# Optimization experiments

Hardware: AMD Instinct MI355X
Metric: run time of the kernel (lower is better)

Reference implementation:

```python
import jax, jax.numpy as jnp
import numpy as np

B, L, D, N, R = 8, 4096, 768, 16, 8

def setup_inputs() -> dict:
    key = jax.random.key(0)
    ks = jax.random.split(key, 12)
    return {
        "x": jax.random.normal(ks[0], (B, L, D), jnp.float32),
        "a_logit": jnp.zeros((N,), jnp.float32),
        "U": jax.random.normal(ks[1], (N, R), jnp.float32) * 0.02,
        "V": jax.random.normal(ks[2], (N, R), jnp.float32) * 0.02,
        "W_in": jax.random.normal(ks[3], (N, D), jnp.float32) * (1.0 / np.sqrt(D)),
        "b_in": jax.random.normal(ks[4], (N,), jnp.float32) * 0.02,
        "W_gate": jax.random.normal(ks[5], (N, D), jnp.float32) * (1.0 / np.sqrt(D)),
        "b_gate": jax.random.normal(ks[6], (N,), jnp.float32) * 0.02,
        "W_out": jax.random.normal(ks[7], (D, N), jnp.float32) * (1.0 / np.sqrt(N)),
        "b_out": jax.random.normal(ks[8], (D,), jnp.float32) * 0.02,
        "W_skip": jax.random.normal(ks[9], (D, D), jnp.float32) * (1.0 / np.sqrt(D)),
        "b_skip": jax.random.normal(ks[10], (D,), jnp.float32) * 0.02,
    }

def reference(x, a_logit, U, V, W_in, b_in, W_gate, b_gate, W_out, b_out, W_skip, b_skip):
    # x: [B, L, D]
    u = jnp.einsum('bld,nd->bln', x, W_in) + b_in            # [B, L, N]
    g = jax.nn.sigmoid(jnp.einsum('bld,nd->bln', x, W_gate) + b_gate)
    a = jax.nn.sigmoid(a_logit)                              # [N]
    lowrank_T = V @ U.T                                      # (U @ V.T).T, [N, N]
    gu = g * u                                               # [B, L, N]

    def step(h, gu_t):
        # h: [B, N]; h_new = a*h + g_t*u_t + h @ lowrank.T
        h = h * a + gu_t + h @ lowrank_T
        return h, h

    h0 = jnp.zeros((x.shape[0], a_logit.shape[0]), x.dtype)
    _, hs = jax.lax.scan(step, h0, jnp.swapaxes(gu, 0, 1))   # hs: [L, B, N]
    hs = jnp.swapaxes(hs, 0, 1)                              # [B, L, N]
    # batched out_proj + skip across all timesteps
    y = jnp.einsum('bln,dn->bld', hs, W_out) + b_out \
        + jnp.einsum('ble,de->bld', x, W_skip) + b_skip
    return y
```

## Files before the change

kernel.cpp:

```cpp
#include <hip/hip_runtime.h>
#include <hip/hip_bf16.h>
#include <math.h>

#define BB 8
#define LL 4096
#define DD 768
#define NN 16
#define RR 8
#define MROWS (BB*LL)
#define KAUG 800
#define CCH 64
#define NCH (LL/CCH)

typedef unsigned int u32;
typedef unsigned short u16;
typedef __attribute__((ext_vector_type(8))) short short8;
typedef __attribute__((ext_vector_type(4))) float f32x4;
typedef __attribute__((ext_vector_type(4))) unsigned short us4;

__device__ __forceinline__ u16 f2bf(float f) {
  u32 u = __float_as_uint(f);
  u32 r = (u + 0x7fffu + ((u >> 16) & 1u)) >> 16;
  return (u16)r;
}

__device__ __forceinline__ void gload_lds16(const void* g, void* l) {
  __builtin_amdgcn_global_load_lds(
      (const __attribute__((address_space(1))) u32*)g,
      (__attribute__((address_space(3))) u32*)l, 16, 0, 0);
}

__global__ void k_prep(const float* __restrict__ a_logit, const float* __restrict__ U,
                       const float* __restrict__ V, const float* __restrict__ b_out,
                       const float* __restrict__ b_skip,
                       float* __restrict__ Mw, float* __restrict__ MCw,
                       float* __restrict__ bsum) {
  __shared__ float cur[256];
  __shared__ float nxt[256];
  int t = threadIdx.x;
  int m = t >> 4, n = t & 15;
  float s = 0.f;
  #pragma unroll
  for (int r = 0; r < RR; r++) s += V[m*RR+r] * U[n*RR+r];
  if (m == n) s += 1.f / (1.f + expf(-a_logit[n]));
  cur[t] = s;
  Mw[t] = s;
  __syncthreads();
  for (int it = 0; it < 6; ++it) {
    float acc = 0.f;
    #pragma unroll
    for (int k = 0; k < 16; k++) acc += cur[m*16+k] * cur[k*16+n];
    nxt[t] = acc;
    __syncthreads();
    cur[t] = nxt[t];
    __syncthreads();
  }
  MCw[t] = cur[t];
  for (int d = t; d < DD; d += 256) bsum[d] = b_out[d] + b_skip[d];
}

__global__ void k_weights(const float* __restrict__ W_skip, const float* __restrict__ W_out,
                          const float* __restrict__ W_in, const float* __restrict__ W_gate,
                          u16* __restrict__ Waug, u16* __restrict__ WinG) {
  int bid = blockIdx.x;
  int t = threadIdx.x;
  if (bid < DD) {
    int d = bid;
    for (int c = t; c < KAUG; c += 256) {
      float v;
      if (c < DD)           v = W_skip[d*DD + c];
      else if (c < DD+NN)   v = W_out[d*NN + (c-DD)];
      else                  v = 0.f;
      Waug[d*KAUG + c] = f2bf(v);
    }
  } else {
    int r = bid - DD;
    const float* Wsrc = (r < NN) ? (W_in + r*DD) : (W_gate + (r-NN)*DD);
    for (int c = t; c < DD; c += 256) WinG[r*DD + c] = f2bf(Wsrc[c]);
  }
}

__global__ void k_convert(const float* __restrict__ x, u16* __restrict__ Xaug) {
  const long total4 = (long)MROWS * (DD/4);
  const int stride = gridDim.x * blockDim.x;
  for (long i = (long)blockIdx.x*blockDim.x + threadIdx.x; i < total4; i += stride) {
    long row = i / (DD/4);
    int  c4  = (int)(i - row*(DD/4));
    float4 v = ((const float4*)x)[i];
    us4 o;
    o.x = f2bf(v.x); o.y = f2bf(v.y); o.z = f2bf(v.z); o.w = f2bf(v.w);
    *(us4*)(Xaug + row*KAUG + c4*4) = o;
  }
  const long totalz = (long)MROWS * 4;
  for (long i = (long)blockIdx.x*blockDim.x + threadIdx.x; i < totalz; i += stride) {
    long row = i >> 2; int q = (int)(i & 3);
    us4 z = (us4)0;
    *(us4*)(Xaug + row*KAUG + 784 + q*4) = z;
  }
}

__global__ __launch_bounds__(256) void k_gu(const u16* __restrict__ Xaug,
                                            const u16* __restrict__ WinG,
                                            const float* __restrict__ b_in,
                                            const float* __restrict__ b_gate,
                                            float* __restrict__ gu) {
  __shared__ u16 At[128*32];
  __shared__ u16 Bt[32*32];
  int tid = threadIdx.x;
  int wave = tid >> 6, lane = tid & 63;
  int rowbase = blockIdx.x * 128;
  f32x4 acc[2][2] = {};
  for (int it = 0; it < DD/32; ++it) {
    int k0 = it * 32;
    #pragma unroll
    for (int p = 0; p < 2; p++) {
      int c = tid + p*256;
      int r = c >> 2, co = c & 3;
      gload_lds16(Xaug + (long)(rowbase + r)*KAUG + k0 + co*8, At + c*8);
    }
    if (tid < 128) {
      int r = tid >> 2, co = tid & 3;
      gload_lds16(WinG + r*DD + k0 + co*8, Bt + tid*8);
    }
    __syncthreads();
    int l15 = lane & 15, lh = lane >> 4;
    short8 a[2], b[2];
    #pragma unroll
    for (int i = 0; i < 2; i++)
      a[i] = *(const short8*)(At + (wave*32 + i*16 + l15)*32 + lh*8);
    #pragma unroll
    for (int j = 0; j < 2; j++)
      b[j] = *(const short8*)(Bt + (j*16 + l15)*32 + lh*8);
    #pragma unroll
    for (int i = 0; i < 2; i++)
      #pragma unroll
      for (int j = 0; j < 2; j++)
        acc[i][j] = __builtin_amdgcn_mfma_f32_16x16x32_bf16(a[i], b[j], acc[i][j], 0, 0, 0);
    __syncthreads();
  }
  int l15 = lane & 15, lh = lane >> 4;
  float bi = b_in[l15], bg = b_gate[l15];
  #pragma unroll
  for (int i = 0; i < 2; i++)
    #pragma unroll
    for (int r = 0; r < 4; r++) {
      int row = rowbase + wave*32 + i*16 + lh*4 + r;
      float u = acc[i][0][r] + bi;
      float g = 1.f / (1.f + __expf(-(acc[i][1][r] + bg)));
      gu[(long)row*NN + l15] = g * u;
    }
}

__global__ void k_scan_local(const float* __restrict__ gu, const float* __restrict__ Mw,
                             float* __restrict__ cend) {
  int lane = threadIdx.x & 63;
  int grp = lane >> 4, n = lane & 15;
  int cid = blockIdx.x*4 + grp;
  int b = cid >> 6, k = cid & 63;
  float Mcol[16];
  #pragma unroll
  for (int m = 0; m < 16; m++) Mcol[m] = Mw[m*16 + n];
  float h = 0.f;
  const float* g = gu + ((long)(b*LL) + k*CCH)*NN + n;
  for (int t = 0; t < CCH; t++) {
    float hn = g[(long)t*NN];
    #pragma unroll
    for (int m = 0; m < 16; m++) hn += __shfl(h, m, 16) * Mcol[m];
    h = hn;
  }
  cend[(b*NCH + k)*NN + n] = h;
}

__global__ void k_scan_prefix(const float* __restrict__ cend, const float* __restrict__ MCw,
                              float* __restrict__ Hstart) {
  int t = threadIdx.x;
  int b = t >> 4, n = t & 15;
  float Mcol[16];
  #pragma unroll
  for (int m = 0; m < 16; m++) Mcol[m] = MCw[m*16 + n];
  float h = 0.f;
  for (int k = 0; k < NCH; k++) {
    Hstart[(b*NCH + k)*NN + n] = h;
    float hn = cend[(b*NCH + k)*NN + n];
    #pragma unroll
    for (int m = 0; m < 16; m++) hn += __shfl(h, m, 16) * Mcol[m];
    h = hn;
  }
}

__global__ void k_scan_final(const float* __restrict__ gu, const float* __restrict__ Mw,
                             const float* __restrict__ Hstart, u16* __restrict__ Xaug) {
  int lane = threadIdx.x & 63;
  int grp = lane >> 4, n = lane & 15;
  int cid = blockIdx.x*4 + grp;
  int b = cid >> 6, k = cid & 63;
  float Mcol[16];
  #pragma unroll
  for (int m = 0; m < 16; m++) Mcol[m] = Mw[m*16 + n];
  float h = Hstart[(b*NCH + k)*NN + n];
  const float* g = gu + ((long)(b*LL) + k*CCH)*NN + n;
  u16* xa = Xaug + ((long)(b*LL) + k*CCH)*KAUG + DD + n;
  for (int t = 0; t < CCH; t++) {
    float hn = g[(long)t*NN];
    #pragma unroll
    for (int m = 0; m < 16; m++) hn += __shfl(h, m, 16) * Mcol[m];
    h = hn;
    xa[(long)t*KAUG] = f2bf(h);
  }
}

__global__ __launch_bounds__(256) void k_out(const u16* __restrict__ Xaug,
                                             const u16* __restrict__ Waug,
                                             const float* __restrict__ bsum,
                                             float* __restrict__ y) {
  __shared__ u16 At[128*32];
  __shared__ u16 Bt[128*32];
  int tid = threadIdx.x;
  int wave = tid >> 6, lane = tid & 63;
  int wm = wave >> 1, wn = wave & 1;
  int rowbase = blockIdx.x * 128;
  int colbase = blockIdx.y * 128;
  f32x4 acc[4][4] = {};
  for (int it = 0; it < KAUG/32; ++it) {
    int k0 = it * 32;
    #pragma unroll
    for (int p = 0; p < 2; p++) {
      int c = tid + p*256;
      int r = c >> 2, co = c & 3;
      gload_lds16(Xaug + (long)(rowbase + r)*KAUG + k0 + co*8, At + c*8);
      gload_lds16(Waug + (long)(colbase + r)*KAUG + k0 + co*8, Bt + c*8);
    }
    __syncthreads();
    int l15 = lane & 15, lh = lane >> 4;
    short8 a[4], b[4];
    #pragma unroll
    for (int i = 0; i < 4; i++)
      a[i] = *(const short8*)(At + (wm*64 + i*16 + l15)*32 + lh*8);
    #pragma unroll
    for (int j = 0; j < 4; j++)
      b[j] = *(const short8*)(Bt + (wn*64 + j*16 + l15)*32 + lh*8);
    #pragma unroll
    for (int i = 0; i < 4; i++)
      #pragma unroll
      for (int j = 0; j < 4; j++)
        acc[i][j] = __builtin_amdgcn_mfma_f32_16x16x32_bf16(a[i], b[j], acc[i][j], 0, 0, 0);
    __syncthreads();
  }
  int l15 = lane & 15, lh = lane >> 4;
  #pragma unroll
  for (int j = 0; j < 4; j++) {
    int col = colbase + wn*64 + j*16 + l15;
    float bs = bsum[col];
    #pragma unroll
    for (int i = 0; i < 4; i++) {
      int row0 = rowbase + wm*64 + i*16 + lh*4;
      #pragma unroll
      for (int r = 0; r < 4; r++)
        y[(long)(row0 + r)*DD + col] = acc[i][j][r] + bs;
    }
  }
}

extern "C" void kernel_launch(void* const* d_in, const int* in_sizes, int n_in,
                              void* d_out, int out_size, void* d_ws, size_t ws_size,
                              hipStream_t stream) {
  (void)in_sizes; (void)n_in; (void)out_size; (void)ws_size;
  const float* x       = (const float*)d_in[0];
  const float* a_logit = (const float*)d_in[1];
  const float* U       = (const float*)d_in[2];
  const float* V       = (const float*)d_in[3];
  const float* W_in    = (const float*)d_in[4];
  const float* b_in    = (const float*)d_in[5];
  const float* W_gate  = (const float*)d_in[6];
  const float* b_gate  = (const float*)d_in[7];
  const float* W_out   = (const float*)d_in[8];
  const float* b_out   = (const float*)d_in[9];
  const float* W_skip  = (const float*)d_in[10];
  const float* b_skip  = (const float*)d_in[11];

  char* ws = (char*)d_ws;
  u16*   Xaug = (u16*)(ws + 0);
  u16*   Waug = (u16*)(ws + 52428800);
  u16*   WinG = (u16*)(ws + 53657600);
  float* gu   = (float*)(ws + 53706752);
  float* Mw   = (float*)(ws + 55803904);
  float* MCw  = (float*)(ws + 55804928);
  float* cend = (float*)(ws + 55805952);
  float* Hst  = (float*)(ws + 55838720);
  float* bsum = (float*)(ws + 55871488);
  float* y    = (float*)d_out;

  hipLaunchKernelGGL(k_prep,        dim3(1),      dim3(256), 0, stream,
                     a_logit, U, V, b_out, b_skip, Mw, MCw, bsum);
  hipLaunchKernelGGL(k_weights,     dim3(800),    dim3(256), 0, stream,
                     W_skip, W_out, W_in, W_gate, Waug, WinG);
  hipLaunchKernelGGL(k_convert,     dim3(2048),   dim3(256), 0, stream, x, Xaug);
  hipLaunchKernelGGL(k_gu,          dim3(256),    dim3(256), 0, stream,
                     Xaug, WinG, b_in, b_gate, gu);
  hipLaunchKernelGGL(k_scan_local,  dim3(128),    dim3(64),  0, stream, gu, Mw, cend);
  hipLaunchKernelGGL(k_scan_prefix, dim3(1),      dim3(128), 0, stream, cend, MCw, Hst);
  hipLaunchKernelGGL(k_scan_final,  dim3(128),    dim3(64),  0, stream, gu, Mw, Hst, Xaug);
  hipLaunchKernelGGL(k_out,         dim3(256, 6), dim3(256), 0, stream,
                     Xaug, Waug, bsum, y);
}
```

Measured before the change: 339.7 us.

## Transpose gu layout, prefetch scan chunks, stage prefix in LDS, swizzle out-GEMM blocks

Writes gu in a time-major transposed layout [B,N,L] so each scan lane reads its 64-step chunk as contiguous float4 loads into registers before the serial recurrence. This removes dependent strided global loads from the latency-bound scan loop. The convert kernel now maps one row per wave instead of using a grid-stride loop with divisions. The prefix scan stages cend in shared memory, and the output GEMM uses a 1D grid with a block swizzle to improve L2 reuse. The risk is extra register pressure from the 64-element gv arrays.

```diff
diff --git a/kernel.cpp b/kernel.cpp
--- a/kernel.cpp
+++ b/kernel.cpp
@@ -81,29 +81,26 @@
 }
 
 __global__ void k_convert(const float* __restrict__ x, u16* __restrict__ Xaug) {
-  const long total4 = (long)MROWS * (DD/4);
-  const int stride = gridDim.x * blockDim.x;
-  for (long i = (long)blockIdx.x*blockDim.x + threadIdx.x; i < total4; i += stride) {
-    long row = i / (DD/4);
-    int  c4  = (int)(i - row*(DD/4));
-    float4 v = ((const float4*)x)[i];
+  int row  = blockIdx.x * 4 + (threadIdx.x >> 6);
+  int lane = threadIdx.x & 63;
+  const float4* xr = (const float4*)(x + (long)row * DD);
+  u16* xo = Xaug + (long)row * KAUG;
+  #pragma unroll
+  for (int p = 0; p < 3; p++) {
+    int c4 = lane + p*64;
+    float4 v = xr[c4];
     us4 o;
     o.x = f2bf(v.x); o.y = f2bf(v.y); o.z = f2bf(v.z); o.w = f2bf(v.w);
-    *(us4*)(Xaug + row*KAUG + c4*4) = o;
-  }
-  const long totalz = (long)MROWS * 4;
-  for (long i = (long)blockIdx.x*blockDim.x + threadIdx.x; i < totalz; i += stride) {
-    long row = i >> 2; int q = (int)(i & 3);
-    us4 z = (us4)0;
-    *(us4*)(Xaug + row*KAUG + 784 + q*4) = z;
-  }
+    *(us4*)(xo + c4*4) = o;
+  }
+  if (lane < 4) *(us4*)(xo + 784 + lane*4) = (us4)0;
 }
 
 __global__ __launch_bounds__(256) void k_gu(const u16* __restrict__ Xaug,
                                             const u16* __restrict__ WinG,
                                             const float* __restrict__ b_in,
                                             const float* __restrict__ b_gate,
-                                            float* __restrict__ gu) {
+                                            float* __restrict__ gu_T) {
   __shared__ u16 At[128*32];
   __shared__ u16 Bt[32*32];
   int tid = threadIdx.x;
@@ -141,17 +138,25 @@
   int l15 = lane & 15, lh = lane >> 4;
   float bi = b_in[l15], bg = b_gate[l15];
   #pragma unroll
-  for (int i = 0; i < 2; i++)
-    #pragma unroll
-    for (int r = 0; r < 4; r++) {
-      int row = rowbase + wave*32 + i*16 + lh*4 + r;
-      float u = acc[i][0][r] + bi;
-      float g = 1.f / (1.f + __expf(-(acc[i][1][r] + bg)));
-      gu[(long)row*NN + l15] = g * u;
-    }
-}
-
-__global__ void k_scan_local(const float* __restrict__ gu, const float* __restrict__ Mw,
+  for (int i = 0; i < 2; i++) {
+    int row0 = rowbase + wave*32 + i*16 + lh*4;
+    int b = row0 >> 12;
+    int t0 = row0 & 4095;
+    float4 o;
+    {
+      float u0 = acc[i][0][0] + bi, u1 = acc[i][0][1] + bi;
+      float u2 = acc[i][0][2] + bi, u3 = acc[i][0][3] + bi;
+      float g0 = 1.f/(1.f+__expf(-(acc[i][1][0]+bg)));
+      float g1 = 1.f/(1.f+__expf(-(acc[i][1][1]+bg)));
+      float g2 = 1.f/(1.f+__expf(-(acc[i][1][2]+bg)));
+      float g3 = 1.f/(1.f+__expf(-(acc[i][1][3]+bg)));
+      o.x = g0*u0; o.y = g1*u1; o.z = g2*u2; o.w = g3*u3;
+    }
+    *(float4*)(gu_T + ((long)(b*16 + l15) << 12) + t0) = o;
+  }
+}
+
+__global__ void k_scan_local(const float* __restrict__ gu_T, const float* __restrict__ Mw,
                              float* __restrict__ cend) {
   int lane = threadIdx.x & 63;
   int grp = lane >> 4, n = lane & 15;
@@ -160,10 +165,17 @@
   float Mcol[16];
   #pragma unroll
   for (int m = 0; m < 16; m++) Mcol[m] = Mw[m*16 + n];
+  const float4* g4 = (const float4*)(gu_T + ((long)(b*16 + n) << 12) + k*CCH);
+  float gv[CCH];
+  #pragma unroll
+  for (int q = 0; q < CCH/4; q++) {
+    float4 v = g4[q];
+    gv[q*4+0]=v.x; gv[q*4+1]=v.y; gv[q*4+2]=v.z; gv[q*4+3]=v.w;
+  }
   float h = 0.f;
-  const float* g = gu + ((long)(b*LL) + k*CCH)*NN + n;
+  #pragma unroll
   for (int t = 0; t < CCH; t++) {
-    float hn = g[(long)t*NN];
+    float hn = gv[t];
     #pragma unroll
     for (int m = 0; m < 16; m++) hn += __shfl(h, m, 16) * Mcol[m];
     h = hn;
@@ -173,22 +185,27 @@
 
 __global__ void k_scan_prefix(const float* __restrict__ cend, const float* __restrict__ MCw,
                               float* __restrict__ Hstart) {
+  __shared__ float s[BB*NCH*NN];
   int t = threadIdx.x;
-  int b = t >> 4, n = t & 15;
-  float Mcol[16];
-  #pragma unroll
-  for (int m = 0; m < 16; m++) Mcol[m] = MCw[m*16 + n];
-  float h = 0.f;
-  for (int k = 0; k < NCH; k++) {
-    Hstart[(b*NCH + k)*NN + n] = h;
-    float hn = cend[(b*NCH + k)*NN + n];
-    #pragma unroll
-    for (int m = 0; m < 16; m++) hn += __shfl(h, m, 16) * Mcol[m];
-    h = hn;
-  }
-}
-
-__global__ void k_scan_final(const float* __restrict__ gu, const float* __restrict__ Mw,
+  for (int i = t; i < BB*NCH*NN; i += 256) s[i] = cend[i];
+  __syncthreads();
+  if (t < 128) {
+    int b = t >> 4, n = t & 15;
+    float Mcol[16];
+    #pragma unroll
+    for (int m = 0; m < 16; m++) Mcol[m] = MCw[m*16 + n];
+    float h = 0.f;
+    for (int k = 0; k < NCH; k++) {
+      Hstart[(b*NCH + k)*NN + n] = h;
+      float hn = s[(b*NCH + k)*NN + n];
+      #pragma unroll
+      for (int m = 0; m < 16; m++) hn += __shfl(h, m, 16) * Mcol[m];
+      h = hn;
+    }
+  }
+}
+
+__global__ void k_scan_final(const float* __restrict__ gu_T, const float* __restrict__ Mw,
                              const float* __restrict__ Hstart, u16* __restrict__ Xaug) {
   int lane = threadIdx.x & 63;
   int grp = lane >> 4, n = lane & 15;
@@ -197,11 +214,18 @@
   float Mcol[16];
   #pragma unroll
   for (int m = 0; m < 16; m++) Mcol[m] = Mw[m*16 + n];
+  const float4* g4 = (const float4*)(gu_T + ((long)(b*16 + n) << 12) + k*CCH);
+  float gv[CCH];
+  #pragma unroll
+  for (int q = 0; q < CCH/4; q++) {
+    float4 v = g4[q];
+    gv[q*4+0]=v.x; gv[q*4+1]=v.y; gv[q*4+2]=v.z; gv[q*4+3]=v.w;
+  }
   float h = Hstart[(b*NCH + k)*NN + n];
-  const float* g = gu + ((long)(b*LL) + k*CCH)*NN + n;
   u16* xa = Xaug + ((long)(b*LL) + k*CCH)*KAUG + DD + n;
+  #pragma unroll
   for (int t = 0; t < CCH; t++) {
-    float hn = g[(long)t*NN];
+    float hn = gv[t];
     #pragma unroll
     for (int m = 0; m < 16; m++) hn += __shfl(h, m, 16) * Mcol[m];
     h = hn;
@@ -218,8 +242,10 @@
   int tid = threadIdx.x;
   int wave = tid >> 6, lane = tid & 63;
   int wm = wave >> 1, wn = wave & 1;
-  int rowbase = blockIdx.x * 128;
-  int colbase = blockIdx.y * 128;
+  int bid = blockIdx.x;
+  int swz = (bid & 7) * 192 + (bid >> 3);
+  int rowbase = (swz & 255) * 128;
+  int colbase = (swz >> 8) * 128;
   f32x4 acc[4][4] = {};
   for (int it = 0; it < KAUG/32; ++it) {
     int k0 = it * 32;
@@ -282,7 +308,7 @@
   u16*   Xaug = (u16*)(ws + 0);
   u16*   Waug = (u16*)(ws + 52428800);
   u16*   WinG = (u16*)(ws + 53657600);
-  float* gu   = (float*)(ws + 53706752);
+  float* gu_T = (float*)(ws + 53706752);
   float* Mw   = (float*)(ws + 55803904);
   float* MCw  = (float*)(ws + 55804928);
   float* cend = (float*)(ws + 55805952);
@@ -290,16 +316,16 @@
   float* bsum = (float*)(ws + 55871488);
   float* y    = (float*)d_out;
 
-  hipLaunchKernelGGL(k_prep,        dim3(1),      dim3(256), 0, stream,
+  hipLaunchKernelGGL(k_prep,        dim3(1),       dim3(256), 0, stream,
                      a_logit, U, V, b_out, b_skip, Mw, MCw, bsum);
-  hipLaunchKernelGGL(k_weights,     dim3(800),    dim3(256), 0, stream,
+  hipLaunchKernelGGL(k_weights,     dim3(800),     dim3(256), 0, stream,
                      W_skip, W_out, W_in, W_gate, Waug, WinG);
-  hipLaunchKernelGGL(k_convert,     dim3(2048),   dim3(256), 0, stream, x, Xaug);
-  hipLaunchKernelGGL(k_gu,          dim3(256),    dim3(256), 0, stream,
-                     Xaug, WinG, b_in, b_gate, gu);
-  hipLaunchKernelGGL(k_scan_local,  dim3(128),    dim3(64),  0, stream, gu, Mw, cend);
-  hipLaunchKernelGGL(k_scan_prefix, dim3(1),      dim3(128), 0, stream, cend, MCw, Hst);
-  hipLaunchKernelGGL(k_scan_final,  dim3(128),    dim3(64),  0, stream, gu, Mw, Hst, Xaug);
-  hipLaunchKernelGGL(k_out,         dim3(256, 6), dim3(256), 0, stream,
+  hipLaunchKernelGGL(k_convert,     dim3(MROWS/4), dim3(256), 0, stream, x, Xaug);
+  hipLaunchKernelGGL(k_gu,          dim3(256),     dim3(256), 0, stream,
+                     Xaug, WinG, b_in, b_gate, gu_T);
+  hipLaunchKernelGGL(k_scan_local,  dim3(128),     dim3(64),  0, stream, gu_T, Mw, cend);
+  hipLaunchKernelGGL(k_scan_prefix, dim3(1),       dim3(256), 0, stream, cend, MCw, Hst);
+  hipLaunchKernelGGL(k_scan_final,  dim3(128),     dim3(64),  0, stream, gu_T, Mw, Hst, Xaug);
+  hipLaunchKernelGGL(k_out,         dim3(1536),    dim3(256), 0, stream,
                      Xaug, Waug, bsum, y);
 }
```

New measurement: 334.2 us. Within noise of the previous version (-1.6%).
